# Kernel tuning notes

Measured on AMD Instinct MI355X. Metric: run time of the kernel, lower is better.

The kernel has to match this reference:

```python
import jax, jax.numpy as jnp
import numpy as np

B, T, H, U, F, K, M = 64, 2048, 1024, 128, 32, 31, 512
PAD = 2 * (K - 1) // 2  # dilation=2, 'same' padding = 30


def setup_inputs() -> dict:
    key = jax.random.key(0)
    ks = jax.random.split(key, 10)
    s = lambda d: 1.0 / np.sqrt(d)
    return {
        "query": jax.random.normal(ks[0], (B, 1, H), dtype=jnp.float32),
        "state": jax.random.uniform(ks[1], (B, T), dtype=jnp.float32),
        "prev_cum": jnp.zeros((B, T), dtype=jnp.float32),
        "memory": jax.random.normal(ks[2], (B, T, M), dtype=jnp.float32),
        "Wq": jax.random.normal(ks[3], (H, U), dtype=jnp.float32) * s(H),
        "bq": jnp.zeros((U,), dtype=jnp.float32),
        "Wm": jax.random.normal(ks[4], (M, U), dtype=jnp.float32) * s(M),
        "bm": jnp.zeros((U,), dtype=jnp.float32),
        "Wl": jax.random.normal(ks[5], (F, U), dtype=jnp.float32) * s(F),
        "bl": jnp.zeros((U,), dtype=jnp.float32),
        "We": jax.random.normal(ks[6], (U, U), dtype=jnp.float32) * s(U),
        "be": jnp.zeros((U,), dtype=jnp.float32),
        "va": jax.random.normal(ks[7], (U,), dtype=jnp.float32),
        "conv_w": jax.random.normal(ks[8], (F, 1, K), dtype=jnp.float32) * s(K),
        "conv_b": jnp.zeros((F,), dtype=jnp.float32),
    }


def reference(query, state, prev_cum, memory, Wq, bq, Wm, bm, Wl, bl, We, be, va, conv_w, conv_b):
    # query projection, keep first time step: [B,1,U]
    pq = (query @ Wq + bq)[:, 0:1, :]
    # processed memory (done in initialize() in torch): [B,T,U]
    pm = memory @ Wm + bm
    # location features: dilated conv over previous alignment, 'same' length
    x = state[:, None, :]  # [B,1,T]
    f = jax.lax.conv_general_dilated(
        x, conv_w, window_strides=(1,), padding=[(PAD, PAD)],
        rhs_dilation=(2,), dimension_numbers=("NCH", "OIH", "NCH"),
    ) + conv_b[None, :, None]                     # [B,F,T]
    pl = jnp.transpose(f, (0, 2, 1)) @ Wl + bl    # [B,T,U]
    # additive energy with extra linear + v_a reduction: [B,T]
    energy = jnp.sum(va * jnp.tanh((pq + pl + pm) @ We + be), axis=2)
    # smoothing (sigmoid) normalization instead of softmax
    sg = jax.nn.sigmoid(energy)
    alignment = sg / jnp.sum(sg, axis=-1, keepdims=True)  # [B,T]
    cum = prev_cum + alignment  # cumulate_weights=True
    # context over PROCESSED memory, matching self.memoery usage: [B,1,U]
    context = cum[:, None, :] @ pm
    return context
```

## Files before the change

kernel.cpp:

```cpp
#include <hip/hip_runtime.h>

#define Bv 64
#define Tv 2048
#define Hv 1024
#define Uv 128
#define Mv 512

typedef __bf16 bf16x8 __attribute__((ext_vector_type(8)));
typedef float f32x4 __attribute__((ext_vector_type(4)));

union U4BF { uint4 u; bf16x8 b; };

#define MFMA(a, b, c) __builtin_amdgcn_mfma_f32_16x16x32_bf16((a), (b), (c), 0, 0, 0)

#define GLOAD_LDS16(g, l) __builtin_amdgcn_global_load_lds( \
    (const __attribute__((address_space(1))) unsigned int*)(g), \
    (__attribute__((address_space(3))) unsigned int*)(l), 16, 0, 0)

__device__ __forceinline__ unsigned short f2bf(float f) {
  __bf16 h = (__bf16)f;
  return __builtin_bit_cast(unsigned short, h);
}
__device__ __forceinline__ float bf2f(unsigned short u) {
  unsigned int x = ((unsigned int)u) << 16;
  return __builtin_bit_cast(float, x);
}
__device__ __forceinline__ unsigned int pack2(unsigned short lo, unsigned short hi) {
  return (unsigned int)lo | ((unsigned int)hi << 16);
}
__device__ __forceinline__ float tanh_fast(float x) {
  float e = __expf(2.0f * x);
  return 1.0f - 2.0f / (e + 1.0f);
}
__device__ __forceinline__ float sigmoid_fast(float x) {
  return 1.0f / (1.0f + __expf(-x));
}

__global__ __launch_bounds__(128) void k1_kernel(const float* __restrict__ query,
                                                 const float* __restrict__ Wq,
                                                 const float* __restrict__ bq,
                                                 const float* __restrict__ Wl,
                                                 const float* __restrict__ bl,
                                                 const float* __restrict__ conv_w,
                                                 const float* __restrict__ conv_b,
                                                 float* __restrict__ pq,
                                                 float* __restrict__ W2,
                                                 float* __restrict__ bias2) {
  const int bx = blockIdx.x;
  const int u = threadIdx.x;
  if (bx < 512) {
    const int b = bx >> 3, c = bx & 7;
    float acc = (c == 0) ? bq[u] : 0.0f;
    const float* q  = query + b * Hv + c * 128;
    const float* wq = Wq + (size_t)c * 128 * Uv;
    #pragma unroll 8
    for (int h = 0; h < 128; ++h) acc = fmaf(q[h], wq[h * Uv + u], acc);
    unsafeAtomicAdd(&pq[b * Uv + u], acc);
  } else {
    float wl[32];
    #pragma unroll
    for (int f = 0; f < 32; ++f) wl[f] = Wl[f * Uv + u];
    for (int k = 0; k < 31; ++k) {
      float acc = 0.0f;
      #pragma unroll
      for (int f = 0; f < 32; ++f) acc = fmaf(conv_w[f * 31 + k], wl[f], acc);
      W2[k * Uv + u] = acc;
    }
    float acc = bl[u];
    #pragma unroll
    for (int f = 0; f < 32; ++f) acc = fmaf(conv_b[f], wl[f], acc);
    bias2[u] = acc;
  }
}

__global__ __launch_bounds__(256) void k2_kernel(const float* __restrict__ pq,
                                                 const float* __restrict__ bias2,
                                                 const float* __restrict__ bm,
                                                 const float* __restrict__ be,
                                                 const float* __restrict__ We,
                                                 const float* __restrict__ W2,
                                                 float* __restrict__ qe,
                                                 float* __restrict__ w3tmp) {
  const int gtid = blockIdx.x * 256 + threadIdx.x;
  const int r = gtid >> 7, n = gtid & 127;
  if (r < 64) {
    float acc = be[n];
    for (int u = 0; u < Uv; ++u)
      acc = fmaf(pq[r * Uv + u] + bias2[u] + bm[u], We[u * Uv + n], acc);
    qe[r * Uv + n] = acc;
  } else {
    const int w = r - 64;
    float acc = 0.0f;
    if (w < 31) {
      for (int u = 0; u < Uv; ++u) acc = fmaf(W2[w * Uv + u], We[u * Uv + n], acc);
    }
    w3tmp[w * Uv + n] = acc;
  }
}

__global__ __launch_bounds__(256) void k3_kernel(const float* __restrict__ Wm,
                                                 const float* __restrict__ We,
                                                 const float* __restrict__ w3tmp,
                                                 unsigned short* __restrict__ WmF,
                                                 unsigned short* __restrict__ WeF,
                                                 unsigned short* __restrict__ W3F) {
  const int gtid = blockIdx.x * 256 + threadIdx.x;
  const int fid = gtid >> 6, lane = gtid & 63;
  const int quad = lane >> 4, l4 = lane & 15;
  float v[8];
  unsigned short* dst;
  if (fid < 128) {
    const int kc = fid >> 3, uj = fid & 7;
    #pragma unroll
    for (int j = 0; j < 8; ++j) v[j] = Wm[(size_t)(kc * 32 + quad * 8 + j) * Uv + uj * 16 + l4];
    dst = WmF + (size_t)fid * 512 + lane * 8;
  } else if (fid < 160) {
    const int f2 = fid - 128;
    const int kc = f2 >> 3, nj = f2 & 7;
    #pragma unroll
    for (int j = 0; j < 8; ++j) v[j] = We[(size_t)(kc * 32 + quad * 8 + j) * Uv + nj * 16 + l4];
    dst = WeF + (size_t)f2 * 512 + lane * 8;
  } else {
    const int nj = fid - 160;
    #pragma unroll
    for (int j = 0; j < 8; ++j) v[j] = w3tmp[(quad * 8 + j) * Uv + nj * 16 + l4];
    dst = W3F + (size_t)nj * 512 + lane * 8;
  }
  uint4 o;
  o.x = pack2(f2bf(v[0]), f2bf(v[1]));
  o.y = pack2(f2bf(v[2]), f2bf(v[3]));
  o.z = pack2(f2bf(v[4]), f2bf(v[5]));
  o.w = pack2(f2bf(v[6]), f2bf(v[7]));
  *(uint4*)dst = o;
}

__global__ __launch_bounds__(256) void ph1_kernel(
    const float* __restrict__ memory, const unsigned short* __restrict__ WmF,
    unsigned short* __restrict__ pm) {
  const int tid = threadIdx.x;
  const int lane = tid & 63, wid = tid >> 6;
  const int l4 = lane & 15, quad = lane >> 4;
  const int wt = wid >> 1, wu = wid & 1;
  const int b = blockIdx.y, t0 = blockIdx.x * 64;

  __shared__ __align__(16) char smem[18432];
  float* sAf = (float*)smem;
  unsigned short* sS = (unsigned short*)smem;

  const int p0 = tid, p1 = tid + 256;
  const int sr0 = p0 >> 3, sc0 = (p0 & 7) ^ (sr0 & 7);
  const int sr1 = p1 >> 3, sc1 = (p1 & 7) ^ (sr1 & 7);
  const float* g0 = memory + ((size_t)b * Tv + t0 + sr0) * Mv + sc0 * 4;
  const float* g1 = memory + ((size_t)b * Tv + t0 + sr1) * Mv + sc1 * 4;

  {
    float* d = sAf + wid * 256;
    GLOAD_LDS16(g0, d); GLOAD_LDS16(g1, d + 1024);
  }

  const int r0 = wt * 32 + l4;
  const int q2 = quad * 2, rx = r0 & 7;
  const int s00 = r0 * 8 + (q2 ^ rx);
  const int s01 = r0 * 8 + ((q2 + 1) ^ rx);

  f32x4 acc[2][4];
  #pragma unroll
  for (int ti = 0; ti < 2; ++ti)
    #pragma unroll
    for (int uj = 0; uj < 4; ++uj) acc[ti][uj] = (f32x4){0.f, 0.f, 0.f, 0.f};

  const unsigned short* bBase = WmF + (size_t)(wu * 4) * 512 + lane * 8;
  uint4 bc0 = *(const uint4*)(bBase);
  uint4 bc1 = *(const uint4*)(bBase + 512);
  uint4 bc2 = *(const uint4*)(bBase + 1024);
  uint4 bc3 = *(const uint4*)(bBase + 1536);

  __syncthreads();

  for (int kc = 0; kc < 16; ++kc) {
    const int cur = kc & 1;
    if (kc < 15) {
      float* d = sAf + (cur ? 0 : 2048) + wid * 256;
      GLOAD_LDS16(g0 + (kc + 1) * 32, d); GLOAD_LDS16(g1 + (kc + 1) * 32, d + 1024);
    }
    uint4 bn0, bn1, bn2, bn3;
    if (kc < 15) {
      const unsigned short* nb = bBase + (size_t)(kc + 1) * 4096;
      bn0 = *(const uint4*)(nb);
      bn1 = *(const uint4*)(nb + 512);
      bn2 = *(const uint4*)(nb + 1024);
      bn3 = *(const uint4*)(nb + 1536);
    }
    const float4* sf = (const float4*)(sAf) + (cur ? 512 : 0);
    float4 a0 = sf[s00];
    float4 a1 = sf[s01];
    float4 a2 = sf[s00 + 128];
    float4 a3 = sf[s01 + 128];
    bf16x8 af0, af1;
    af0[0] = (__bf16)a0.x; af0[1] = (__bf16)a0.y; af0[2] = (__bf16)a0.z; af0[3] = (__bf16)a0.w;
    af0[4] = (__bf16)a1.x; af0[5] = (__bf16)a1.y; af0[6] = (__bf16)a1.z; af0[7] = (__bf16)a1.w;
    af1[0] = (__bf16)a2.x; af1[1] = (__bf16)a2.y; af1[2] = (__bf16)a2.z; af1[3] = (__bf16)a2.w;
    af1[4] = (__bf16)a3.x; af1[5] = (__bf16)a3.y; af1[6] = (__bf16)a3.z; af1[7] = (__bf16)a3.w;
    U4BF u0, u1, u2, u3;
    u0.u = bc0; u1.u = bc1; u2.u = bc2; u3.u = bc3;
    acc[0][0] = MFMA(af0, u0.b, acc[0][0]);
    acc[1][0] = MFMA(af1, u0.b, acc[1][0]);
    acc[0][1] = MFMA(af0, u1.b, acc[0][1]);
    acc[1][1] = MFMA(af1, u1.b, acc[1][1]);
    acc[0][2] = MFMA(af0, u2.b, acc[0][2]);
    acc[1][2] = MFMA(af1, u2.b, acc[1][2]);
    acc[0][3] = MFMA(af0, u3.b, acc[0][3]);
    acc[1][3] = MFMA(af1, u3.b, acc[1][3]);
    if (kc < 15) {
      bc0 = bn0; bc1 = bn1; bc2 = bn2; bc3 = bn3;
      __syncthreads();
    }
  }

  __syncthreads();

  #pragma unroll
  for (int ti = 0; ti < 2; ++ti) {
    const int rowb = wt * 32 + ti * 16 + quad * 4;
    #pragma unroll
    for (int uj = 0; uj < 4; ++uj) {
      const int col = wu * 64 + uj * 16 + l4;
      #pragma unroll
      for (int r = 0; r < 4; ++r) sS[(rowb + r) * 144 + col] = f2bf(acc[ti][uj][r]);
    }
  }
  __syncthreads();

  const size_t baseT = (size_t)b * Tv + t0;
  #pragma unroll
  for (int i = 0; i < 4; ++i) {
    const int idx = i * 256 + tid;
    const int row = idx >> 4, c = idx & 15;
    *(uint4*)&pm[(baseT + row) * Uv + c * 8] = *(const uint4*)&sS[row * 144 + c * 8];
  }
}

__global__ __launch_bounds__(256) void ph23_kernel(
    const unsigned short* __restrict__ pm, const unsigned short* __restrict__ WeF,
    const unsigned short* __restrict__ W3F, const float* __restrict__ qe,
    const float* __restrict__ state, const float* __restrict__ prev_cum,
    const float* __restrict__ bm, const float* __restrict__ va,
    float* __restrict__ P0, float* __restrict__ P1, float* __restrict__ Ssg) {
  const int tid = threadIdx.x;
  const int lane = tid & 63, wid = tid >> 6;
  const int l4 = lane & 15, quad = lane >> 4;
  const int wt = wid >> 1, wu = wid & 1;
  const int b = blockIdx.y, t0 = blockIdx.x * 64;

  __shared__ float sState[124];
  __shared__ float sPc[64];
  __shared__ float sBm[128];
  __shared__ float sVa[128];
  __shared__ float sSg[64];
  __shared__ float blkP0[128], blkP1[128];
  __shared__ float blkSsg;
  __shared__ __align__(16) unsigned short sS[64 * 144];

  for (int i = tid; i < 124; i += 256) {
    int t = t0 - 30 + i;
    sState[i] = (t >= 0 && t < Tv) ? state[b * Tv + t] : 0.0f;
  }
  if (tid < 64) sPc[tid] = prev_cum[b * Tv + t0 + tid];
  for (int i = tid; i < 128; i += 256) {
    sBm[i] = bm[i]; sVa[i] = va[i]; blkP0[i] = 0.0f; blkP1[i] = 0.0f;
  }
  if (tid == 0) blkSsg = 0.0f;

  const size_t baseT = (size_t)b * Tv + t0;
  #pragma unroll
  for (int i = 0; i < 4; ++i) {
    const int idx = i * 256 + tid;
    const int row = idx >> 4, c = idx & 15;
    *(uint4*)&sS[row * 144 + c * 8] = *(const uint4*)&pm[(baseT + row) * Uv + c * 8];
  }
  __syncthreads();

  const int w = wid;
  f32x4 e[8];
  #pragma unroll
  for (int nj = 0; nj < 8; ++nj) {
    float qv = qe[b * Uv + nj * 16 + l4];
    e[nj] = (f32x4){qv, qv, qv, qv};
  }
  bf16x8 a2f;
  #pragma unroll
  for (int j = 0; j < 8; ++j) {
    int k = quad * 8 + j;
    float v = (k < 31) ? sState[(w * 16 + l4) + 2 * k] : 0.0f;
    a2f[j] = (__bf16)v;
  }
  #pragma unroll
  for (int nj = 0; nj < 8; ++nj) {
    U4BF bb; bb.u = *(const uint4*)(W3F + (size_t)nj * 512 + lane * 8);
    e[nj] = MFMA(a2f, bb.b, e[nj]);
  }
  #pragma unroll
  for (int ks = 0; ks < 4; ++ks) {
    U4BF au;
    au.u = *(const uint4*)&sS[(w * 16 + l4) * 144 + ks * 32 + quad * 8];
    #pragma unroll
    for (int nj = 0; nj < 8; ++nj) {
      U4BF bb; bb.u = *(const uint4*)(WeF + (size_t)(ks * 8 + nj) * 512 + lane * 8);
      e[nj] = MFMA(au.b, bb.b, e[nj]);
    }
  }
  float p[4] = {0.f, 0.f, 0.f, 0.f};
  #pragma unroll
  for (int nj = 0; nj < 8; ++nj) {
    float vav = sVa[nj * 16 + l4];
    #pragma unroll
    for (int r = 0; r < 4; ++r) p[r] = fmaf(vav, tanh_fast(e[nj][r]), p[r]);
  }
  #pragma unroll
  for (int off = 1; off <= 8; off <<= 1) {
    #pragma unroll
    for (int r = 0; r < 4; ++r) p[r] += __shfl_xor(p[r], off, 64);
  }
  float sgv4[4], sgsum = 0.f;
  #pragma unroll
  for (int r = 0; r < 4; ++r) {
    sgv4[r] = sigmoid_fast(p[r]);
    sgsum += sgv4[r];
  }
  if (l4 == 0) {
    #pragma unroll
    for (int r = 0; r < 4; ++r) sSg[w * 16 + quad * 4 + r] = sgv4[r];
    atomicAdd(&blkSsg, sgsum);
  }
  __syncthreads();

  float sgl[8], pcl[8];
  #pragma unroll
  for (int ti = 0; ti < 2; ++ti)
    #pragma unroll
    for (int r = 0; r < 4; ++r) {
      int row = wt * 32 + ti * 16 + quad * 4 + r;
      sgl[ti * 4 + r] = sSg[row];
      pcl[ti * 4 + r] = sPc[row];
    }
  #pragma unroll
  for (int uj = 0; uj < 4; ++uj) {
    const int col = wu * 64 + uj * 16 + l4;
    const float bmv = sBm[col];
    float c0 = 0.f, c1 = 0.f;
    #pragma unroll
    for (int ti = 0; ti < 2; ++ti)
      #pragma unroll
      for (int r = 0; r < 4; ++r) {
        const int row = wt * 32 + ti * 16 + quad * 4 + r;
        float pmv = bf2f(sS[row * 144 + col]) + bmv;
        c0 = fmaf(pcl[ti * 4 + r], pmv, c0);
        c1 = fmaf(sgl[ti * 4 + r], pmv, c1);
      }
    c0 += __shfl_xor(c0, 16, 64); c0 += __shfl_xor(c0, 32, 64);
    c1 += __shfl_xor(c1, 16, 64); c1 += __shfl_xor(c1, 32, 64);
    if (quad == 0) {
      atomicAdd(&blkP0[col], c0);
      atomicAdd(&blkP1[col], c1);
    }
  }
  __syncthreads();
  if (tid < 128) {
    unsafeAtomicAdd(&P0[b * Uv + tid], blkP0[tid]);
    unsafeAtomicAdd(&P1[b * Uv + tid], blkP1[tid]);
  }
  if (tid == 0) unsafeAtomicAdd(&Ssg[b], blkSsg);
}

__global__ __launch_bounds__(128) void finish_kernel(const float* __restrict__ P0,
                                                     const float* __restrict__ P1,
                                                     const float* __restrict__ Ssg,
                                                     float* __restrict__ out) {
  const int b = blockIdx.x, u = threadIdx.x;
  out[b * Uv + u] = P0[b * Uv + u] + P1[b * Uv + u] / Ssg[b];
}

extern "C" void kernel_launch(void* const* d_in, const int* in_sizes, int n_in,
                              void* d_out, int out_size, void* d_ws, size_t ws_size,
                              hipStream_t stream) {
  (void)in_sizes; (void)n_in; (void)out_size; (void)ws_size;
  const float* query    = (const float*)d_in[0];
  const float* state    = (const float*)d_in[1];
  const float* prev_cum = (const float*)d_in[2];
  const float* memory   = (const float*)d_in[3];
  const float* Wq       = (const float*)d_in[4];
  const float* bq       = (const float*)d_in[5];
  const float* Wm       = (const float*)d_in[6];
  const float* bm       = (const float*)d_in[7];
  const float* Wl       = (const float*)d_in[8];
  const float* bl       = (const float*)d_in[9];
  const float* We       = (const float*)d_in[10];
  const float* be       = (const float*)d_in[11];
  const float* va       = (const float*)d_in[12];
  const float* conv_w   = (const float*)d_in[13];
  const float* conv_b   = (const float*)d_in[14];

  float* ws = (float*)d_ws;
  float* P0    = ws;
  float* P1    = ws + 8192;
  float* Ssg   = ws + 16384;
  float* pq    = ws + 16448;
  float* W2    = ws + 24640;
  float* bias2 = ws + 28608;
  float* qe    = ws + 28736;
  float* w3tmp = ws + 36928;
  unsigned short* WmF = (unsigned short*)(ws + 41024);
  unsigned short* WeF = (unsigned short*)(ws + 73792);
  unsigned short* W3F = (unsigned short*)(ws + 81984);
  unsigned short* pm  = (unsigned short*)(ws + 84032);

  hipMemsetAsync(d_ws, 0, 24640 * sizeof(float), stream);

  k1_kernel<<<513, 128, 0, stream>>>(query, Wq, bq, Wl, bl, conv_w, conv_b, pq, W2, bias2);
  k2_kernel<<<48, 256, 0, stream>>>(pq, bias2, bm, be, We, W2, qe, w3tmp);
  k3_kernel<<<42, 256, 0, stream>>>(Wm, We, w3tmp, WmF, WeF, W3F);
  ph1_kernel<<<dim3(Tv / 64, Bv), 256, 0, stream>>>(memory, WmF, pm);
  ph23_kernel<<<dim3(Tv / 64, Bv), 256, 0, stream>>>(
      pm, WeF, W3F, qe, state, prev_cum, bm, va, P0, P1, Ssg);
  finish_kernel<<<Bv, 128, 0, stream>>>(P0, P1, Ssg, (float*)d_out);
}
```

Measured before the change: 453.4 us.

## Fuse memory projection with energy/context phase and merge preprocessing kernels

Merges the memory projection (ph1) and the energy/context kernel (ph23) into a single main kernel, so the bf16 processed-memory tile stays in LDS and registers instead of going through a global round trip. The context accumulation now reads pm straight from the fp32 MFMA accumulators. The three small preprocessing kernels and the memset are folded into one kpre kernel, which also zeroes the accumulators. The per-batch query-energy GEMV (qe) is moved into every main-kernel block, adding redundant work of 128x128 FMAs per block with uncoalesced-ish We reads.

```diff
diff --git a/kernel.cpp b/kernel.cpp
--- a/kernel.cpp
+++ b/kernel.cpp
@@ -21,10 +21,6 @@
   __bf16 h = (__bf16)f;
   return __builtin_bit_cast(unsigned short, h);
 }
-__device__ __forceinline__ float bf2f(unsigned short u) {
-  unsigned int x = ((unsigned int)u) << 16;
-  return __builtin_bit_cast(float, x);
-}
 __device__ __forceinline__ unsigned int pack2(unsigned short lo, unsigned short hi) {
   return (unsigned int)lo | ((unsigned int)hi << 16);
 }
@@ -36,113 +32,130 @@
   return 1.0f / (1.0f + __expf(-x));
 }
 
-__global__ __launch_bounds__(128) void k1_kernel(const float* __restrict__ query,
-                                                 const float* __restrict__ Wq,
-                                                 const float* __restrict__ bq,
-                                                 const float* __restrict__ Wl,
-                                                 const float* __restrict__ bl,
-                                                 const float* __restrict__ conv_w,
-                                                 const float* __restrict__ conv_b,
-                                                 float* __restrict__ pq,
-                                                 float* __restrict__ W2,
-                                                 float* __restrict__ bias2) {
-  const int bx = blockIdx.x;
-  const int u = threadIdx.x;
-  if (bx < 512) {
-    const int b = bx >> 3, c = bx & 7;
-    float acc = (c == 0) ? bq[u] : 0.0f;
-    const float* q  = query + b * Hv + c * 128;
-    const float* wq = Wq + (size_t)c * 128 * Uv;
+__global__ __launch_bounds__(256) void kpre_kernel(
+    const float* __restrict__ query, const float* __restrict__ Wq,
+    const float* __restrict__ bq, const float* __restrict__ Wl,
+    const float* __restrict__ bl, const float* __restrict__ conv_w,
+    const float* __restrict__ conv_b, const float* __restrict__ Wm,
+    const float* __restrict__ We,
+    float* __restrict__ pq, float* __restrict__ bias2,
+    unsigned short* __restrict__ WmF, unsigned short* __restrict__ WeF,
+    unsigned short* __restrict__ W3F,
+    float* __restrict__ P0, float* __restrict__ P1, float* __restrict__ Ssg) {
+  const int bx = blockIdx.x, tid = threadIdx.x;
+
+  if (bx < 64) {
+    __shared__ float sTmp[2][128];
+    const int b = bx;
+    const int u = tid & 127, half = tid >> 7;
+    float acc = 0.0f;
+    const float* q  = query + b * Hv + half * 512;
+    const float* wq = Wq + (size_t)half * 512 * Uv + u;
     #pragma unroll 8
-    for (int h = 0; h < 128; ++h) acc = fmaf(q[h], wq[h * Uv + u], acc);
-    unsafeAtomicAdd(&pq[b * Uv + u], acc);
+    for (int h = 0; h < 512; ++h) acc = fmaf(q[h], wq[(size_t)h * Uv], acc);
+    sTmp[half][u] = acc;
+    if (tid < 128) P0[b * Uv + tid] = 0.0f;
+    else           P1[b * Uv + (tid - 128)] = 0.0f;
+    if (tid == 0) Ssg[b] = 0.0f;
+    __syncthreads();
+    if (tid < 128) pq[b * Uv + tid] = sTmp[0][tid] + sTmp[1][tid] + bq[tid];
+  } else if (bx == 64) {
+    __shared__ float sW2[31][128];
+    __shared__ float sW3[32][128];
+    if (tid < 128) {
+      const int u = tid;
+      float wl[32];
+      #pragma unroll
+      for (int f = 0; f < 32; ++f) wl[f] = Wl[f * Uv + u];
+      for (int k = 0; k < 31; ++k) {
+        float acc = 0.0f;
+        #pragma unroll
+        for (int f = 0; f < 32; ++f) acc = fmaf(conv_w[f * 31 + k], wl[f], acc);
+        sW2[k][u] = acc;
+      }
+      float acc = bl[u];
+      #pragma unroll
+      for (int f = 0; f < 32; ++f) acc = fmaf(conv_b[f], wl[f], acc);
+      bias2[u] = acc;
+    }
+    __syncthreads();
+    if (tid < 128) {
+      const int n = tid;
+      for (int w = 0; w < 32; ++w) {
+        float acc = 0.0f;
+        if (w < 31) {
+          for (int uu = 0; uu < Uv; ++uu)
+            acc = fmaf(sW2[w][uu], We[(size_t)uu * Uv + n], acc);
+        }
+        sW3[w][n] = acc;
+      }
+    }
+    __syncthreads();
+    #pragma unroll
+    for (int i = 0; i < 2; ++i) {
+      const int idx = i * 256 + tid;
+      const int nj = idx >> 6, lane = idx & 63;
+      const int quad = lane >> 4, l4 = lane & 15;
+      float v[8];
+      #pragma unroll
+      for (int j = 0; j < 8; ++j) v[j] = sW3[quad * 8 + j][nj * 16 + l4];
+      uint4 o;
+      o.x = pack2(f2bf(v[0]), f2bf(v[1]));
+      o.y = pack2(f2bf(v[2]), f2bf(v[3]));
+      o.z = pack2(f2bf(v[4]), f2bf(v[5]));
+      o.w = pack2(f2bf(v[6]), f2bf(v[7]));
+      *(uint4*)(W3F + (size_t)nj * 512 + lane * 8) = o;
+    }
   } else {
-    float wl[32];
-    #pragma unroll
-    for (int f = 0; f < 32; ++f) wl[f] = Wl[f * Uv + u];
-    for (int k = 0; k < 31; ++k) {
-      float acc = 0.0f;
-      #pragma unroll
-      for (int f = 0; f < 32; ++f) acc = fmaf(conv_w[f * 31 + k], wl[f], acc);
-      W2[k * Uv + u] = acc;
-    }
-    float acc = bl[u];
-    #pragma unroll
-    for (int f = 0; f < 32; ++f) acc = fmaf(conv_b[f], wl[f], acc);
-    bias2[u] = acc;
-  }
-}
-
-__global__ __launch_bounds__(256) void k2_kernel(const float* __restrict__ pq,
-                                                 const float* __restrict__ bias2,
-                                                 const float* __restrict__ bm,
-                                                 const float* __restrict__ be,
-                                                 const float* __restrict__ We,
-                                                 const float* __restrict__ W2,
-                                                 float* __restrict__ qe,
-                                                 float* __restrict__ w3tmp) {
-  const int gtid = blockIdx.x * 256 + threadIdx.x;
-  const int r = gtid >> 7, n = gtid & 127;
-  if (r < 64) {
-    float acc = be[n];
-    for (int u = 0; u < Uv; ++u)
-      acc = fmaf(pq[r * Uv + u] + bias2[u] + bm[u], We[u * Uv + n], acc);
-    qe[r * Uv + n] = acc;
-  } else {
-    const int w = r - 64;
-    float acc = 0.0f;
-    if (w < 31) {
-      for (int u = 0; u < Uv; ++u) acc = fmaf(W2[w * Uv + u], We[u * Uv + n], acc);
-    }
-    w3tmp[w * Uv + n] = acc;
-  }
-}
-
-__global__ __launch_bounds__(256) void k3_kernel(const float* __restrict__ Wm,
-                                                 const float* __restrict__ We,
-                                                 const float* __restrict__ w3tmp,
-                                                 unsigned short* __restrict__ WmF,
-                                                 unsigned short* __restrict__ WeF,
-                                                 unsigned short* __restrict__ W3F) {
-  const int gtid = blockIdx.x * 256 + threadIdx.x;
-  const int fid = gtid >> 6, lane = gtid & 63;
-  const int quad = lane >> 4, l4 = lane & 15;
-  float v[8];
-  unsigned short* dst;
-  if (fid < 128) {
-    const int kc = fid >> 3, uj = fid & 7;
-    #pragma unroll
-    for (int j = 0; j < 8; ++j) v[j] = Wm[(size_t)(kc * 32 + quad * 8 + j) * Uv + uj * 16 + l4];
-    dst = WmF + (size_t)fid * 512 + lane * 8;
-  } else if (fid < 160) {
-    const int f2 = fid - 128;
-    const int kc = f2 >> 3, nj = f2 & 7;
-    #pragma unroll
-    for (int j = 0; j < 8; ++j) v[j] = We[(size_t)(kc * 32 + quad * 8 + j) * Uv + nj * 16 + l4];
-    dst = WeF + (size_t)f2 * 512 + lane * 8;
-  } else {
-    const int nj = fid - 160;
-    #pragma unroll
-    for (int j = 0; j < 8; ++j) v[j] = w3tmp[(quad * 8 + j) * Uv + nj * 16 + l4];
-    dst = W3F + (size_t)nj * 512 + lane * 8;
-  }
-  uint4 o;
-  o.x = pack2(f2bf(v[0]), f2bf(v[1]));
-  o.y = pack2(f2bf(v[2]), f2bf(v[3]));
-  o.z = pack2(f2bf(v[4]), f2bf(v[5]));
-  o.w = pack2(f2bf(v[6]), f2bf(v[7]));
-  *(uint4*)dst = o;
-}
-
-__global__ __launch_bounds__(256) void ph1_kernel(
+    const int fid = (bx - 65) * 4 + (tid >> 6);
+    const int lane = tid & 63;
+    const int quad = lane >> 4, l4 = lane & 15;
+    float v[8];
+    unsigned short* dst;
+    if (fid < 128) {
+      const int kc = fid >> 3, uj = fid & 7;
+      #pragma unroll
+      for (int j = 0; j < 8; ++j) v[j] = Wm[(size_t)(kc * 32 + quad * 8 + j) * Uv + uj * 16 + l4];
+      dst = WmF + (size_t)fid * 512 + lane * 8;
+    } else {
+      const int f2 = fid - 128;
+      const int kc = f2 >> 3, nj = f2 & 7;
+      #pragma unroll
+      for (int j = 0; j < 8; ++j) v[j] = We[(size_t)(kc * 32 + quad * 8 + j) * Uv + nj * 16 + l4];
+      dst = WeF + (size_t)f2 * 512 + lane * 8;
+    }
+    uint4 o;
+    o.x = pack2(f2bf(v[0]), f2bf(v[1]));
+    o.y = pack2(f2bf(v[2]), f2bf(v[3]));
+    o.z = pack2(f2bf(v[4]), f2bf(v[5]));
+    o.w = pack2(f2bf(v[6]), f2bf(v[7]));
+    *(uint4*)dst = o;
+  }
+}
+
+__global__ __launch_bounds__(256) void main_kernel(
     const float* __restrict__ memory, const unsigned short* __restrict__ WmF,
-    unsigned short* __restrict__ pm) {
+    const unsigned short* __restrict__ WeF, const unsigned short* __restrict__ W3F,
+    const float* __restrict__ pq, const float* __restrict__ bias2,
+    const float* __restrict__ be, const float* __restrict__ We,
+    const float* __restrict__ state, const float* __restrict__ prev_cum,
+    const float* __restrict__ bm, const float* __restrict__ va,
+    float* __restrict__ P0, float* __restrict__ P1, float* __restrict__ Ssg) {
   const int tid = threadIdx.x;
   const int lane = tid & 63, wid = tid >> 6;
   const int l4 = lane & 15, quad = lane >> 4;
   const int wt = wid >> 1, wu = wid & 1;
   const int b = blockIdx.y, t0 = blockIdx.x * 64;
 
+  __shared__ float sState[124];
+  __shared__ float sPc[64];
+  __shared__ float sBm[128];
+  __shared__ float sVa[128];
+  __shared__ float sSg[64];
+  __shared__ float blkP0[128], blkP1[128];
+  __shared__ float blkSsg;
+  __shared__ float sQin[128];
+  __shared__ float sQe[128];
   __shared__ __align__(16) char smem[18432];
   float* sAf = (float*)smem;
   unsigned short* sS = (unsigned short*)smem;
@@ -158,24 +171,42 @@
     GLOAD_LDS16(g0, d); GLOAD_LDS16(g1, d + 1024);
   }
 
-  const int r0 = wt * 32 + l4;
-  const int q2 = quad * 2, rx = r0 & 7;
-  const int s00 = r0 * 8 + (q2 ^ rx);
-  const int s01 = r0 * 8 + ((q2 + 1) ^ rx);
-
-  f32x4 acc[2][4];
-  #pragma unroll
-  for (int ti = 0; ti < 2; ++ti)
-    #pragma unroll
-    for (int uj = 0; uj < 4; ++uj) acc[ti][uj] = (f32x4){0.f, 0.f, 0.f, 0.f};
-
   const unsigned short* bBase = WmF + (size_t)(wu * 4) * 512 + lane * 8;
   uint4 bc0 = *(const uint4*)(bBase);
   uint4 bc1 = *(const uint4*)(bBase + 512);
   uint4 bc2 = *(const uint4*)(bBase + 1024);
   uint4 bc3 = *(const uint4*)(bBase + 1536);
 
-  __syncthreads();
+  for (int i = tid; i < 124; i += 256) {
+    int t = t0 - 30 + i;
+    sState[i] = (t >= 0 && t < Tv) ? state[b * Tv + t] : 0.0f;
+  }
+  if (tid < 64) sPc[tid] = prev_cum[b * Tv + t0 + tid];
+  for (int i = tid; i < 128; i += 256) {
+    float bmv = bm[i];
+    sBm[i] = bmv; sVa[i] = va[i]; blkP0[i] = 0.0f; blkP1[i] = 0.0f;
+    sQin[i] = pq[b * Uv + i] + bias2[i] + bmv;
+  }
+  if (tid == 0) blkSsg = 0.0f;
+
+  const int r0 = wt * 32 + l4;
+  const int q2 = quad * 2, rx = r0 & 7;
+  const int s00 = r0 * 8 + (q2 ^ rx);
+  const int s01 = r0 * 8 + ((q2 + 1) ^ rx);
+
+  f32x4 acc[2][4];
+  #pragma unroll
+  for (int ti = 0; ti < 2; ++ti)
+    #pragma unroll
+    for (int uj = 0; uj < 4; ++uj) acc[ti][uj] = (f32x4){0.f, 0.f, 0.f, 0.f};
+
+  __syncthreads();
+
+  if (tid < 128) {
+    float acc_q = be[tid];
+    for (int u = 0; u < Uv; ++u) acc_q = fmaf(sQin[u], We[(size_t)u * Uv + tid], acc_q);
+    sQe[tid] = acc_q;
+  }
 
   for (int kc = 0; kc < 16; ++kc) {
     const int cur = kc & 1;
@@ -231,60 +262,11 @@
   }
   __syncthreads();
 
-  const size_t baseT = (size_t)b * Tv + t0;
-  #pragma unroll
-  for (int i = 0; i < 4; ++i) {
-    const int idx = i * 256 + tid;
-    const int row = idx >> 4, c = idx & 15;
-    *(uint4*)&pm[(baseT + row) * Uv + c * 8] = *(const uint4*)&sS[row * 144 + c * 8];
-  }
-}
-
-__global__ __launch_bounds__(256) void ph23_kernel(
-    const unsigned short* __restrict__ pm, const unsigned short* __restrict__ WeF,
-    const unsigned short* __restrict__ W3F, const float* __restrict__ qe,
-    const float* __restrict__ state, const float* __restrict__ prev_cum,
-    const float* __restrict__ bm, const float* __restrict__ va,
-    float* __restrict__ P0, float* __restrict__ P1, float* __restrict__ Ssg) {
-  const int tid = threadIdx.x;
-  const int lane = tid & 63, wid = tid >> 6;
-  const int l4 = lane & 15, quad = lane >> 4;
-  const int wt = wid >> 1, wu = wid & 1;
-  const int b = blockIdx.y, t0 = blockIdx.x * 64;
-
-  __shared__ float sState[124];
-  __shared__ float sPc[64];
-  __shared__ float sBm[128];
-  __shared__ float sVa[128];
-  __shared__ float sSg[64];
-  __shared__ float blkP0[128], blkP1[128];
-  __shared__ float blkSsg;
-  __shared__ __align__(16) unsigned short sS[64 * 144];
-
-  for (int i = tid; i < 124; i += 256) {
-    int t = t0 - 30 + i;
-    sState[i] = (t >= 0 && t < Tv) ? state[b * Tv + t] : 0.0f;
-  }
-  if (tid < 64) sPc[tid] = prev_cum[b * Tv + t0 + tid];
-  for (int i = tid; i < 128; i += 256) {
-    sBm[i] = bm[i]; sVa[i] = va[i]; blkP0[i] = 0.0f; blkP1[i] = 0.0f;
-  }
-  if (tid == 0) blkSsg = 0.0f;
-
-  const size_t baseT = (size_t)b * Tv + t0;
-  #pragma unroll
-  for (int i = 0; i < 4; ++i) {
-    const int idx = i * 256 + tid;
-    const int row = idx >> 4, c = idx & 15;
-    *(uint4*)&sS[row * 144 + c * 8] = *(const uint4*)&pm[(baseT + row) * Uv + c * 8];
-  }
-  __syncthreads();
-
   const int w = wid;
   f32x4 e[8];
   #pragma unroll
   for (int nj = 0; nj < 8; ++nj) {
-    float qv = qe[b * Uv + nj * 16 + l4];
+    float qv = sQe[nj * 16 + l4];
     e[nj] = (f32x4){qv, qv, qv, qv};
   }
   bf16x8 a2f;
@@ -352,8 +334,7 @@
     for (int ti = 0; ti < 2; ++ti)
       #pragma unroll
       for (int r = 0; r < 4; ++r) {
-        const int row = wt * 32 + ti * 16 + quad * 4 + r;
-        float pmv = bf2f(sS[row * 144 + col]) + bmv;
+        float pmv = acc[ti][uj][r] + bmv;
         c0 = fmaf(pcl[ti * 4 + r], pmv, c0);
         c1 = fmaf(sgl[ti * 4 + r], pmv, c1);
       }
@@ -405,22 +386,14 @@
   float* P1    = ws + 8192;
   float* Ssg   = ws + 16384;
   float* pq    = ws + 16448;
-  float* W2    = ws + 24640;
   float* bias2 = ws + 28608;
-  float* qe    = ws + 28736;
-  float* w3tmp = ws + 36928;
   unsigned short* WmF = (unsigned short*)(ws + 41024);
   unsigned short* WeF = (unsigned short*)(ws + 73792);
   unsigned short* W3F = (unsigned short*)(ws + 81984);
-  unsigned short* pm  = (unsigned short*)(ws + 84032);
-
-  hipMemsetAsync(d_ws, 0, 24640 * sizeof(float), stream);
-
-  k1_kernel<<<513, 128, 0, stream>>>(query, Wq, bq, Wl, bl, conv_w, conv_b, pq, W2, bias2);
-  k2_kernel<<<48, 256, 0, stream>>>(pq, bias2, bm, be, We, W2, qe, w3tmp);
-  k3_kernel<<<42, 256, 0, stream>>>(Wm, We, w3tmp, WmF, WeF, W3F);
-  ph1_kernel<<<dim3(Tv / 64, Bv), 256, 0, stream>>>(memory, WmF, pm);
-  ph23_kernel<<<dim3(Tv / 64, Bv), 256, 0, stream>>>(
-      pm, WeF, W3F, qe, state, prev_cum, bm, va, P0, P1, Ssg);
+
+  kpre_kernel<<<105, 256, 0, stream>>>(query, Wq, bq, Wl, bl, conv_w, conv_b, Wm, We,
+                                       pq, bias2, WmF, WeF, W3F, P0, P1, Ssg);
+  main_kernel<<<dim3(Tv / 64, Bv), 256, 0, stream>>>(
+      memory, WmF, WeF, W3F, pq, bias2, be, We, state, prev_cum, bm, va, P0, P1, Ssg);
   finish_kernel<<<Bv, 128, 0, stream>>>(P0, P1, Ssg, (float*)d_out);
 }
```

Measured after the change: 511.4 us. +12.8%, slower.
